# Performance work log

Measured on AMD Instinct MI355X. Metric: run time of the kernel, lower is better.

## Reference

```python
import jax, jax.numpy as jnp
import numpy as np

N_NODES = 50000
N_EDGES = 800000
F_IN = 128
HID = 128
N_CLASSES = 2
N_GRAPHS = 500
NEG_SLOPE = 0.2


def setup_inputs() -> dict:
    key = jax.random.key(0)
    ks = jax.random.split(key, 16)
    inp = {
        "x": jax.random.normal(ks[0], (N_NODES, F_IN), dtype=jnp.float32),
        "edge_index": jax.random.randint(ks[1], (2, N_EDGES), 0, N_NODES, dtype=jnp.int64),
        "batch": jnp.sort(jax.random.randint(ks[2], (N_NODES,), 0, N_GRAPHS, dtype=jnp.int64)),
    }
    dims = [(F_IN, HID), (HID, HID), (HID, HID)]
    for i, (din, dout) in enumerate(dims, start=1):
        s = 1.0 / np.sqrt(din)
        inp[f"W{i}"] = jax.random.uniform(ks[3 * i], (din, dout), minval=-s, maxval=s, dtype=jnp.float32)
        inp[f"a_src{i}"] = jax.random.uniform(ks[3 * i + 1], (dout,), minval=-s, maxval=s, dtype=jnp.float32)
        inp[f"a_dst{i}"] = jax.random.uniform(ks[3 * i + 2], (dout,), minval=-s, maxval=s, dtype=jnp.float32)
        inp[f"b{i}"] = jnp.zeros((dout,), dtype=jnp.float32)
    s = 1.0 / np.sqrt(HID)
    inp["W_lin"] = jax.random.uniform(ks[12], (HID, N_CLASSES), minval=-s, maxval=s, dtype=jnp.float32)
    inp["b_lin"] = jax.random.uniform(ks[13], (N_CLASSES,), minval=-s, maxval=s, dtype=jnp.float32)
    return inp


def gat_conv(x, src, dst, W, a_src, a_dst, b, n_nodes):
    # single-head PyG GATConv (heads=1, concat), self-loops already in src/dst
    h = x @ W                                   # [N, dout]
    alpha_src = h @ a_src                       # [N]
    alpha_dst = h @ a_dst                       # [N]
    e = jax.nn.leaky_relu(alpha_src[src] + alpha_dst[dst], NEG_SLOPE)  # [E]
    # segment softmax over edges grouped by destination node
    m = jax.ops.segment_max(e, dst, num_segments=n_nodes)
    ex = jnp.exp(e - m[dst])
    denom = jax.ops.segment_sum(ex, dst, num_segments=n_nodes)
    alpha = ex / denom[dst]                     # [E]
    out = jax.ops.segment_sum(h[src] * alpha[:, None], dst, num_segments=n_nodes)
    return out + b


def reference(x, edge_index, batch, W1, a_src1, a_dst1, b1, W2, a_src2, a_dst2, b2,
              W3, a_src3, a_dst3, b3, W_lin, b_lin):
    n = x.shape[0]
    loops = jnp.arange(n, dtype=edge_index.dtype)
    src = jnp.concatenate([edge_index[0], loops])
    dst = jnp.concatenate([edge_index[1], loops])

    h = jax.nn.relu(gat_conv(x, src, dst, W1, a_src1, a_dst1, b1, n))
    h = jax.nn.relu(gat_conv(h, src, dst, W2, a_src2, a_dst2, b2, n))
    h = gat_conv(h, src, dst, W3, a_src3, a_dst3, b3, n)

    # global mean pool over graphs
    sums = jax.ops.segment_sum(h, batch, num_segments=N_GRAPHS)       # [G, HID]
    counts = jax.ops.segment_sum(jnp.ones((n,), h.dtype), batch, num_segments=N_GRAPHS)
    pooled = sums / jnp.maximum(counts, 1.0)[:, None]
    # dropout is identity in eval mode
    return pooled @ W_lin + b_lin
```

## Files before the change

### kernel.cpp

```cpp
#include <hip/hip_runtime.h>
#include <math.h>

#define N_NODES  50000
#define N_EDGES  800000
#define FDIM     128
#define N_GRAPHS 500
#define NEG_SLOPE 0.2f
#define EN_TOTAL (N_EDGES + N_NODES)
#define SCAN_NB ((N_NODES + 255) / 256)
#define GEMM_TILES (N_NODES / 16)

typedef short bf16x8 __attribute__((ext_vector_type(8)));
typedef float f32x4 __attribute__((ext_vector_type(4)));

static __device__ __forceinline__ float lrelu(float x) {
    return x >= 0.f ? x : NEG_SLOPE * x;
}
static __device__ __forceinline__ unsigned short f2bf(float v) {
    unsigned int u = __float_as_uint(v);
    u += 0x7fffu + ((u >> 16) & 1u);
    return (unsigned short)(u >> 16);
}
static __device__ __forceinline__ float bf2f(unsigned short s) {
    return __uint_as_float(((unsigned int)s) << 16);
}

__global__ __launch_bounds__(256) void prep_planes(
    const float* __restrict__ X, unsigned short* __restrict__ hi,
    unsigned short* __restrict__ lo)
{
    const int total = N_NODES * FDIM / 4;
    for (int i = blockIdx.x * 256 + threadIdx.x; i < total; i += gridDim.x * 256) {
        const float4 v = ((const float4*)X)[i];
        ushort4 h4, l4;
        h4.x = f2bf(v.x); l4.x = f2bf(v.x - bf2f(h4.x));
        h4.y = f2bf(v.y); l4.y = f2bf(v.y - bf2f(h4.y));
        h4.z = f2bf(v.z); l4.z = f2bf(v.z - bf2f(h4.z));
        h4.w = f2bf(v.w); l4.w = f2bf(v.w - bf2f(h4.w));
        ((ushort4*)hi)[i] = h4;
        ((ushort4*)lo)[i] = l4;
    }
}

__global__ __launch_bounds__(256) void prep_wt(
    const float* __restrict__ W0, const float* __restrict__ W1,
    const float* __restrict__ W2, unsigned short* __restrict__ WT)
{
    const float* W = (blockIdx.x == 0) ? W0 : (blockIdx.x == 1) ? W1 : W2;
    unsigned short* hi = WT + (size_t)blockIdx.x * 2 * FDIM * FDIM;
    unsigned short* lo = hi + FDIM * FDIM;
    for (int i = threadIdx.x; i < FDIM * FDIM; i += 256) {
        const int k = i >> 7, c = i & 127;
        const float v = W[i];
        const unsigned short h = f2bf(v);
        hi[c * FDIM + k] = h;
        lo[c * FDIM + k] = f2bf(v - bf2f(h));
    }
}

__global__ __launch_bounds__(256) void gemm_mfma3(
    const unsigned short* __restrict__ Ahi, const unsigned short* __restrict__ Alo,
    const unsigned short* __restrict__ WThi, const unsigned short* __restrict__ WTlo,
    const float* __restrict__ Avs, const float* __restrict__ Avd,
    unsigned short* __restrict__ Hb, float* __restrict__ asrcN, float* __restrict__ adstN)
{
    __shared__ float sps[4][16], spd[4][16];

    const int tid = threadIdx.x, wv = tid >> 6, lane = tid & 63;
    const int r16 = lane & 15, g = lane >> 4;
    const int t0 = wv * 2;

    bf16x8 bh[2][4], bl[2][4];
    float as_v[2], ad_v[2];
    #pragma unroll
    for (int tt = 0; tt < 2; ++tt) {
        const int c = (t0 + tt) * 16 + r16;
        as_v[tt] = Avs[c];
        ad_v[tt] = Avd[c];
        #pragma unroll
        for (int cc = 0; cc < 4; ++cc) {
            bh[tt][cc] = *(const bf16x8*)(WThi + c * FDIM + cc * 32 + 8 * g);
            bl[tt][cc] = *(const bf16x8*)(WTlo + c * FDIM + cc * 32 + 8 * g);
        }
    }

    for (int tile = blockIdx.x; tile < GEMM_TILES; tile += gridDim.x) {
        const int m0 = tile * 16;
        const size_t ra = (size_t)(m0 + r16) * FDIM;

        f32x4 acc0 = {0.f, 0.f, 0.f, 0.f}, acc1 = {0.f, 0.f, 0.f, 0.f};
        #pragma unroll
        for (int cc = 0; cc < 4; ++cc) {
            const int k0 = cc * 32 + 8 * g;
            const bf16x8 ah = *(const bf16x8*)(Ahi + ra + k0);
            const bf16x8 al = *(const bf16x8*)(Alo + ra + k0);
            acc0 = __builtin_amdgcn_mfma_f32_16x16x32_bf16(ah, bh[0][cc], acc0, 0, 0, 0);
            acc1 = __builtin_amdgcn_mfma_f32_16x16x32_bf16(ah, bh[1][cc], acc1, 0, 0, 0);
            acc0 = __builtin_amdgcn_mfma_f32_16x16x32_bf16(al, bh[0][cc], acc0, 0, 0, 0);
            acc1 = __builtin_amdgcn_mfma_f32_16x16x32_bf16(al, bh[1][cc], acc1, 0, 0, 0);
            acc0 = __builtin_amdgcn_mfma_f32_16x16x32_bf16(ah, bl[0][cc], acc0, 0, 0, 0);
            acc1 = __builtin_amdgcn_mfma_f32_16x16x32_bf16(ah, bl[1][cc], acc1, 0, 0, 0);
        }

        float ps[4], pd[4];
        const int rowb = m0 + 4 * g;
        #pragma unroll
        for (int r = 0; r < 4; ++r) {
            const float h0 = acc0[r], h1 = acc1[r];
            Hb[(size_t)(rowb + r) * FDIM + (t0 + 0) * 16 + r16] = f2bf(h0);
            Hb[(size_t)(rowb + r) * FDIM + (t0 + 1) * 16 + r16] = f2bf(h1);
            ps[r] = h0 * as_v[0] + h1 * as_v[1];
            pd[r] = h0 * ad_v[0] + h1 * ad_v[1];
        }
        #pragma unroll
        for (int o = 1; o <= 8; o <<= 1) {
            #pragma unroll
            for (int r = 0; r < 4; ++r) {
                ps[r] += __shfl_xor(ps[r], o);
                pd[r] += __shfl_xor(pd[r], o);
            }
        }
        if (r16 == 0) {
            #pragma unroll
            for (int r = 0; r < 4; ++r) {
                sps[wv][4 * g + r] = ps[r];
                spd[wv][4 * g + r] = pd[r];
            }
        }
        __syncthreads();
        if (tid < 16) {
            asrcN[m0 + tid] = sps[0][tid] + sps[1][tid] + sps[2][tid] + sps[3][tid];
        } else if (tid < 32) {
            const int r = tid - 16;
            adstN[m0 + r] = spd[0][r] + spd[1][r] + spd[2][r] + spd[3][r];
        }
        __syncthreads();
    }
}

__global__ void count_edges(const int* __restrict__ ei, int* __restrict__ cnt) {
    int i = blockIdx.x * 256 + threadIdx.x;
    if (i < EN_TOTAL) {
        int d = (i < N_EDGES) ? ei[N_EDGES + i] : (i - N_EDGES);
        atomicAdd(&cnt[d], 1);
    }
}

__global__ __launch_bounds__(256) void scan_block(const int* __restrict__ cnt,
                                                  int* __restrict__ off,
                                                  int* __restrict__ blockSums) {
    __shared__ int s[256];
    const int i = blockIdx.x * 256 + threadIdx.x;
    s[threadIdx.x] = (i < N_NODES) ? cnt[i] : 0;
    __syncthreads();
    #pragma unroll
    for (int d = 1; d < 256; d <<= 1) {
        int t = (threadIdx.x >= d) ? s[threadIdx.x - d] : 0;
        __syncthreads();
        s[threadIdx.x] += t;
        __syncthreads();
    }
    if (i < N_NODES) off[i + 1] = s[threadIdx.x];
    if (threadIdx.x == 255) blockSums[blockIdx.x] = s[255];
}

__global__ __launch_bounds__(256) void scan_sums(int* __restrict__ blockSums) {
    __shared__ int s[256];
    s[threadIdx.x] = (threadIdx.x < SCAN_NB) ? blockSums[threadIdx.x] : 0;
    __syncthreads();
    #pragma unroll
    for (int d = 1; d < 256; d <<= 1) {
        int t = (threadIdx.x >= d) ? s[threadIdx.x - d] : 0;
        __syncthreads();
        s[threadIdx.x] += t;
        __syncthreads();
    }
    if (threadIdx.x < SCAN_NB)
        blockSums[threadIdx.x] = (threadIdx.x == 0) ? 0 : s[threadIdx.x - 1];
}

__global__ __launch_bounds__(256) void add_base(int* __restrict__ off,
                                                const int* __restrict__ blockSums) {
    const int i = blockIdx.x * 256 + threadIdx.x;
    if (i < N_NODES) off[i + 1] += blockSums[blockIdx.x];
    if (i == 0) off[0] = 0;
}

__global__ void scatter_edges(const int* __restrict__ ei, const int* __restrict__ off,
                              int* __restrict__ cur, int* __restrict__ srcs) {
    int i = blockIdx.x * 256 + threadIdx.x;
    if (i < EN_TOTAL) {
        int s, d;
        if (i < N_EDGES) { s = ei[i]; d = ei[N_EDGES + i]; }
        else             { s = d = i - N_EDGES; }
        int p = off[d] + atomicAdd(&cur[d], 1);
        srcs[p] = s;
    }
}

__global__ __launch_bounds__(256) void gat_aggregate(
    const unsigned short* __restrict__ Hb, const int* __restrict__ off,
    const int* __restrict__ srcs,
    const float* __restrict__ asrcN, const float* __restrict__ adstN,
    const float* __restrict__ bias,
    unsigned short* __restrict__ PHI, unsigned short* __restrict__ PLO,
    float* __restrict__ OUTF, int mode)
{
    const int wave = threadIdx.x >> 6, lane = threadIdx.x & 63;
    const int grp = lane >> 3, fl = lane & 7;

    for (int n = blockIdx.x * 4 + wave; n < N_NODES; n += gridDim.x * 4) {
        const int s0 = off[n], s1 = off[n + 1];
        const int deg = s1 - s0;
        const float ad = adstN[n];

        float e_reg = -1e30f;
        float m = -1e30f;
        for (int j = s0 + lane; j < s1; j += 64) {
            float e = lrelu(asrcN[srcs[j]] + ad);
            if (j - s0 < 64) e_reg = e;
            m = fmaxf(m, e);
        }
        #pragma unroll
        for (int o = 32; o; o >>= 1) m = fmaxf(m, __shfl_xor(m, o));

        float4 a0 = {0,0,0,0}, a1 = {0,0,0,0}, a2 = {0,0,0,0}, a3 = {0,0,0,0};
        float dn = 0.f;
        const unsigned short* Hf = Hb + (size_t)fl * 16;
        for (int j = s0 + grp; j < s1; j += 8) {
            const int s = srcs[j];
            const float ex = (deg <= 64)
                ? __expf(__shfl(e_reg, j - s0) - m)
                : __expf(lrelu(asrcN[s] + ad) - m);
            dn += ex;
            const uint4* hp = (const uint4*)(Hf + (size_t)s * FDIM);
            const uint4 u0 = hp[0], u1 = hp[1];
            a0.x += ex * __uint_as_float(u0.x << 16);
            a0.y += ex * __uint_as_float(u0.x & 0xffff0000u);
            a0.z += ex * __uint_as_float(u0.y << 16);
            a0.w += ex * __uint_as_float(u0.y & 0xffff0000u);
            a1.x += ex * __uint_as_float(u0.z << 16);
            a1.y += ex * __uint_as_float(u0.z & 0xffff0000u);
            a1.z += ex * __uint_as_float(u0.w << 16);
            a1.w += ex * __uint_as_float(u0.w & 0xffff0000u);
            a2.x += ex * __uint_as_float(u1.x << 16);
            a2.y += ex * __uint_as_float(u1.x & 0xffff0000u);
            a2.z += ex * __uint_as_float(u1.y << 16);
            a2.w += ex * __uint_as_float(u1.y & 0xffff0000u);
            a3.x += ex * __uint_as_float(u1.z << 16);
            a3.y += ex * __uint_as_float(u1.z & 0xffff0000u);
            a3.z += ex * __uint_as_float(u1.w << 16);
            a3.w += ex * __uint_as_float(u1.w & 0xffff0000u);
        }

        #pragma unroll
        for (int o = 8; o <= 32; o <<= 1) {
            dn  += __shfl_xor(dn, o);
            a0.x += __shfl_xor(a0.x, o); a0.y += __shfl_xor(a0.y, o);
            a0.z += __shfl_xor(a0.z, o); a0.w += __shfl_xor(a0.w, o);
            a1.x += __shfl_xor(a1.x, o); a1.y += __shfl_xor(a1.y, o);
            a1.z += __shfl_xor(a1.z, o); a1.w += __shfl_xor(a1.w, o);
            a2.x += __shfl_xor(a2.x, o); a2.y += __shfl_xor(a2.y, o);
            a2.z += __shfl_xor(a2.z, o); a2.w += __shfl_xor(a2.w, o);
            a3.x += __shfl_xor(a3.x, o); a3.y += __shfl_xor(a3.y, o);
            a3.z += __shfl_xor(a3.z, o); a3.w += __shfl_xor(a3.w, o);
        }

        if (grp == 0) {
            const float rd = 1.f / dn;
            const float4* bp = (const float4*)(bias + fl * 16);
            float4 ov[4] = {a0, a1, a2, a3};
            #pragma unroll
            for (int q = 0; q < 4; ++q) {
                const float4 b4 = bp[q];
                float4 o4;
                o4.x = ov[q].x * rd + b4.x; o4.y = ov[q].y * rd + b4.y;
                o4.z = ov[q].z * rd + b4.z; o4.w = ov[q].w * rd + b4.w;
                if (mode == 0) {
                    o4.x = fmaxf(o4.x, 0.f); o4.y = fmaxf(o4.y, 0.f);
                    o4.z = fmaxf(o4.z, 0.f); o4.w = fmaxf(o4.w, 0.f);
                    ushort4 h4, l4;
                    h4.x = f2bf(o4.x); l4.x = f2bf(o4.x - bf2f(h4.x));
                    h4.y = f2bf(o4.y); l4.y = f2bf(o4.y - bf2f(h4.y));
                    h4.z = f2bf(o4.z); l4.z = f2bf(o4.z - bf2f(h4.z));
                    h4.w = f2bf(o4.w); l4.w = f2bf(o4.w - bf2f(h4.w));
                    const size_t base = (size_t)n * FDIM + fl * 16 + q * 4;
                    *(ushort4*)(PHI + base) = h4;
                    *(ushort4*)(PLO + base) = l4;
                } else {
                    *(float4*)(OUTF + (size_t)n * FDIM + fl * 16 + q * 4) = o4;
                }
            }
        }
    }
}

__global__ __launch_bounds__(256) void pool_linear2(
    const float* __restrict__ H, const int* __restrict__ batch,
    const float* __restrict__ Wlin, const float* __restrict__ blin,
    float* __restrict__ out)
{
    const int g = blockIdx.x, tid = threadIdx.x;
    const int rl = tid >> 5, fq = tid & 31;

    int a = 0, b = N_NODES;
    while (a < b) { int mid = (a + b) >> 1; if (batch[mid] < g) a = mid + 1; else b = mid; }
    const int lo = a;
    b = N_NODES;
    while (a < b) { int mid = (a + b) >> 1; if (batch[mid] <= g) a = mid + 1; else b = mid; }
    const int hi = a;

    float4 acc = {0.f, 0.f, 0.f, 0.f};
    for (int n = lo + rl; n < hi; n += 8) {
        const float4 v = *(const float4*)(H + (size_t)n * FDIM + fq * 4);
        acc.x += v.x; acc.y += v.y; acc.z += v.z; acc.w += v.w;
    }
    __shared__ float4 s[8][32];
    s[rl][fq] = acc;
    __syncthreads();

    if (tid < 32) {
        float4 t = s[0][fq];
        #pragma unroll
        for (int r = 1; r < 8; ++r) {
            const float4 v = s[r][fq];
            t.x += v.x; t.y += v.y; t.z += v.z; t.w += v.w;
        }
        const float inv = 1.f / fmaxf((float)(hi - lo), 1.f);
        t.x *= inv; t.y *= inv; t.z *= inv; t.w *= inv;
        float d0 = t.x * Wlin[(fq * 4 + 0) * 2 + 0] + t.y * Wlin[(fq * 4 + 1) * 2 + 0]
                 + t.z * Wlin[(fq * 4 + 2) * 2 + 0] + t.w * Wlin[(fq * 4 + 3) * 2 + 0];
        float d1 = t.x * Wlin[(fq * 4 + 0) * 2 + 1] + t.y * Wlin[(fq * 4 + 1) * 2 + 1]
                 + t.z * Wlin[(fq * 4 + 2) * 2 + 1] + t.w * Wlin[(fq * 4 + 3) * 2 + 1];
        #pragma unroll
        for (int o = 1; o <= 16; o <<= 1) {
            d0 += __shfl_xor(d0, o);
            d1 += __shfl_xor(d1, o);
        }
        if (fq == 0) {
            out[g * 2 + 0] = d0 + blin[0];
            out[g * 2 + 1] = d1 + blin[1];
        }
    }
}

extern "C" void kernel_launch(void* const* d_in, const int* in_sizes, int n_in,
                              void* d_out, int out_size, void* d_ws, size_t ws_size,
                              hipStream_t stream)
{
    const float* x     = (const float*)d_in[0];
    const int*   ei    = (const int*)d_in[1];
    const int*   batch = (const int*)d_in[2];
    const float* W[3]    = {(const float*)d_in[3],  (const float*)d_in[7],  (const float*)d_in[11]};
    const float* avs[3]  = {(const float*)d_in[4],  (const float*)d_in[8],  (const float*)d_in[12]};
    const float* avd[3]  = {(const float*)d_in[5],  (const float*)d_in[9],  (const float*)d_in[13]};
    const float* bias[3] = {(const float*)d_in[6],  (const float*)d_in[10], (const float*)d_in[14]};
    const float* Wlin = (const float*)d_in[15];
    const float* blin = (const float*)d_in[16];
    float* out = (float*)d_out;

    char* w = (char*)d_ws;
    unsigned short* Ahi = (unsigned short*)w; w += (size_t)N_NODES * FDIM * 2;
    unsigned short* Alo = (unsigned short*)w; w += (size_t)N_NODES * FDIM * 2;
    float* hOf = (float*)Ahi;
    unsigned short* Hb = (unsigned short*)w; w += (size_t)N_NODES * FDIM * 2;
    float* attn  = (float*)w; w += 2 * 200192;
    int*   off   = (int*)w;   w += 200192;
    int*   cnt   = (int*)w;   w += 200192;
    int*   bsum  = (int*)w;   w += 4096;
    int*   srcs  = (int*)w;   w += (size_t)EN_TOTAL * 4;
    unsigned short* WT = (unsigned short*)w; w += 3 * 2 * FDIM * FDIM * 2;
    float* asrcN = attn;
    float* adstN = attn + N_NODES;

    prep_planes<<<1024, 256, 0, stream>>>(x, Ahi, Alo);
    prep_wt<<<3, 256, 0, stream>>>(W[0], W[1], W[2], WT);

    hipMemsetAsync(cnt, 0, N_NODES * sizeof(int), stream);
    count_edges<<<(EN_TOTAL + 255) / 256, 256, 0, stream>>>(ei, cnt);
    scan_block<<<SCAN_NB, 256, 0, stream>>>(cnt, off, bsum);
    scan_sums<<<1, 256, 0, stream>>>(bsum);
    add_base<<<SCAN_NB, 256, 0, stream>>>(off, bsum);
    hipMemsetAsync(cnt, 0, N_NODES * sizeof(int), stream);
    scatter_edges<<<(EN_TOTAL + 255) / 256, 256, 0, stream>>>(ei, off, cnt, srcs);

    for (int l = 0; l < 3; ++l) {
        const unsigned short* WThi = WT + (size_t)l * 2 * FDIM * FDIM;
        const unsigned short* WTlo = WThi + FDIM * FDIM;
        gemm_mfma3<<<1024, 256, 0, stream>>>(Ahi, Alo, WThi, WTlo,
                                             avs[l], avd[l], Hb, asrcN, adstN);
        gat_aggregate<<<2048, 256, 0, stream>>>(Hb, off, srcs, asrcN, adstN, bias[l],
                                                Ahi, Alo, hOf, (l < 2) ? 0 : 1);
    }

    pool_linear2<<<N_GRAPHS, 256, 0, stream>>>(hOf, batch, Wlin, blin, out);
}
```

Measured before the change: 352.4 us.

## Fold attention vectors into GEMM as extra columns, drop block reduction and syncs

Precomputes W·a_src and W·a_dst in prep_wt and appends them as extra transposed weight columns (padded to 144). One wave per tile, rotated across tiles, computes the attention logits with an extra set of MFMAs. This replaces the shuffle reduction, the shared-memory partial sums and two __syncthreads per tile. The A fragments are also loaded up front. Reassociating the attention dot products through bf16 split planes changes rounding slightly, and the work is unbalanced across waves.

```diff
diff --git a/kernel.cpp b/kernel.cpp
--- a/kernel.cpp
+++ b/kernel.cpp
@@ -9,6 +9,7 @@
 #define EN_TOTAL (N_EDGES + N_NODES)
 #define SCAN_NB ((N_NODES + 255) / 256)
 #define GEMM_TILES (N_NODES / 16)
+#define WT_COLS 144
 
 typedef short bf16x8 __attribute__((ext_vector_type(8)));
 typedef float f32x4 __attribute__((ext_vector_type(4)));
@@ -44,97 +45,120 @@
 
 __global__ __launch_bounds__(256) void prep_wt(
     const float* __restrict__ W0, const float* __restrict__ W1,
-    const float* __restrict__ W2, unsigned short* __restrict__ WT)
-{
-    const float* W = (blockIdx.x == 0) ? W0 : (blockIdx.x == 1) ? W1 : W2;
-    unsigned short* hi = WT + (size_t)blockIdx.x * 2 * FDIM * FDIM;
-    unsigned short* lo = hi + FDIM * FDIM;
-    for (int i = threadIdx.x; i < FDIM * FDIM; i += 256) {
+    const float* __restrict__ W2,
+    const float* __restrict__ as0, const float* __restrict__ as1,
+    const float* __restrict__ as2,
+    const float* __restrict__ ad0, const float* __restrict__ ad1,
+    const float* __restrict__ ad2,
+    unsigned short* __restrict__ WT)
+{
+    const int l = blockIdx.x;
+    const float* W  = (l == 0) ? W0  : (l == 1) ? W1  : W2;
+    const float* As = (l == 0) ? as0 : (l == 1) ? as1 : as2;
+    const float* Ad = (l == 0) ? ad0 : (l == 1) ? ad1 : ad2;
+    unsigned short* hi = WT + (size_t)l * 2 * WT_COLS * FDIM;
+    unsigned short* lo = hi + WT_COLS * FDIM;
+    const int tid = threadIdx.x;
+
+    __shared__ float wa[256];
+    {
+        const int k = tid & 127;
+        const float* av = (tid < 128) ? As : Ad;
+        float s = 0.f;
+        for (int c = 0; c < 128; ++c) s += W[k * FDIM + c] * av[c];
+        wa[tid] = s;
+    }
+    __syncthreads();
+
+    for (int i = tid; i < FDIM * FDIM; i += 256) {
         const int k = i >> 7, c = i & 127;
         const float v = W[i];
         const unsigned short h = f2bf(v);
         hi[c * FDIM + k] = h;
         lo[c * FDIM + k] = f2bf(v - bf2f(h));
     }
-}
-
-__global__ __launch_bounds__(256) void gemm_mfma3(
+    for (int k = tid; k < FDIM; k += 256) {
+        const float vs = wa[k], vd = wa[128 + k];
+        const unsigned short hs = f2bf(vs), hd = f2bf(vd);
+        hi[128 * FDIM + k] = hs; lo[128 * FDIM + k] = f2bf(vs - bf2f(hs));
+        hi[129 * FDIM + k] = hd; lo[129 * FDIM + k] = f2bf(vd - bf2f(hd));
+    }
+    for (int i = tid; i < 14 * FDIM; i += 256) {
+        hi[130 * FDIM + i] = 0;
+        lo[130 * FDIM + i] = 0;
+    }
+}
+
+__global__ __launch_bounds__(256) void gemm_mfma4(
     const unsigned short* __restrict__ Ahi, const unsigned short* __restrict__ Alo,
     const unsigned short* __restrict__ WThi, const unsigned short* __restrict__ WTlo,
-    const float* __restrict__ Avs, const float* __restrict__ Avd,
     unsigned short* __restrict__ Hb, float* __restrict__ asrcN, float* __restrict__ adstN)
 {
-    __shared__ float sps[4][16], spd[4][16];
-
     const int tid = threadIdx.x, wv = tid >> 6, lane = tid & 63;
     const int r16 = lane & 15, g = lane >> 4;
     const int t0 = wv * 2;
 
     bf16x8 bh[2][4], bl[2][4];
-    float as_v[2], ad_v[2];
     #pragma unroll
     for (int tt = 0; tt < 2; ++tt) {
         const int c = (t0 + tt) * 16 + r16;
-        as_v[tt] = Avs[c];
-        ad_v[tt] = Avd[c];
         #pragma unroll
         for (int cc = 0; cc < 4; ++cc) {
             bh[tt][cc] = *(const bf16x8*)(WThi + c * FDIM + cc * 32 + 8 * g);
             bl[tt][cc] = *(const bf16x8*)(WTlo + c * FDIM + cc * 32 + 8 * g);
         }
     }
-
-    for (int tile = blockIdx.x; tile < GEMM_TILES; tile += gridDim.x) {
+    const unsigned short* WThiE = WThi + (128 + r16) * FDIM + 8 * g;
+    const unsigned short* WTloE = WTlo + (128 + r16) * FDIM + 8 * g;
+
+    int rot = 0;
+    for (int tile = blockIdx.x; tile < GEMM_TILES; tile += gridDim.x, ++rot) {
         const int m0 = tile * 16;
         const size_t ra = (size_t)(m0 + r16) * FDIM;
 
+        bf16x8 ah[4], al[4];
+        #pragma unroll
+        for (int cc = 0; cc < 4; ++cc) {
+            ah[cc] = *(const bf16x8*)(Ahi + ra + cc * 32 + 8 * g);
+            al[cc] = *(const bf16x8*)(Alo + ra + cc * 32 + 8 * g);
+        }
+
         f32x4 acc0 = {0.f, 0.f, 0.f, 0.f}, acc1 = {0.f, 0.f, 0.f, 0.f};
         #pragma unroll
         for (int cc = 0; cc < 4; ++cc) {
-            const int k0 = cc * 32 + 8 * g;
-            const bf16x8 ah = *(const bf16x8*)(Ahi + ra + k0);
-            const bf16x8 al = *(const bf16x8*)(Alo + ra + k0);
-            acc0 = __builtin_amdgcn_mfma_f32_16x16x32_bf16(ah, bh[0][cc], acc0, 0, 0, 0);
-            acc1 = __builtin_amdgcn_mfma_f32_16x16x32_bf16(ah, bh[1][cc], acc1, 0, 0, 0);
-            acc0 = __builtin_amdgcn_mfma_f32_16x16x32_bf16(al, bh[0][cc], acc0, 0, 0, 0);
-            acc1 = __builtin_amdgcn_mfma_f32_16x16x32_bf16(al, bh[1][cc], acc1, 0, 0, 0);
-            acc0 = __builtin_amdgcn_mfma_f32_16x16x32_bf16(ah, bl[0][cc], acc0, 0, 0, 0);
-            acc1 = __builtin_amdgcn_mfma_f32_16x16x32_bf16(ah, bl[1][cc], acc1, 0, 0, 0);
-        }
-
-        float ps[4], pd[4];
+            acc0 = __builtin_amdgcn_mfma_f32_16x16x32_bf16(ah[cc], bh[0][cc], acc0, 0, 0, 0);
+            acc1 = __builtin_amdgcn_mfma_f32_16x16x32_bf16(ah[cc], bh[1][cc], acc1, 0, 0, 0);
+            acc0 = __builtin_amdgcn_mfma_f32_16x16x32_bf16(al[cc], bh[0][cc], acc0, 0, 0, 0);
+            acc1 = __builtin_amdgcn_mfma_f32_16x16x32_bf16(al[cc], bh[1][cc], acc1, 0, 0, 0);
+            acc0 = __builtin_amdgcn_mfma_f32_16x16x32_bf16(ah[cc], bl[0][cc], acc0, 0, 0, 0);
+            acc1 = __builtin_amdgcn_mfma_f32_16x16x32_bf16(ah[cc], bl[1][cc], acc1, 0, 0, 0);
+        }
+
         const int rowb = m0 + 4 * g;
         #pragma unroll
         for (int r = 0; r < 4; ++r) {
-            const float h0 = acc0[r], h1 = acc1[r];
-            Hb[(size_t)(rowb + r) * FDIM + (t0 + 0) * 16 + r16] = f2bf(h0);
-            Hb[(size_t)(rowb + r) * FDIM + (t0 + 1) * 16 + r16] = f2bf(h1);
-            ps[r] = h0 * as_v[0] + h1 * as_v[1];
-            pd[r] = h0 * ad_v[0] + h1 * ad_v[1];
-        }
-        #pragma unroll
-        for (int o = 1; o <= 8; o <<= 1) {
+            Hb[(size_t)(rowb + r) * FDIM + (t0 + 0) * 16 + r16] = f2bf(acc0[r]);
+            Hb[(size_t)(rowb + r) * FDIM + (t0 + 1) * 16 + r16] = f2bf(acc1[r]);
+        }
+
+        if (wv == ((tile + rot) & 3)) {
+            f32x4 acce = {0.f, 0.f, 0.f, 0.f};
             #pragma unroll
-            for (int r = 0; r < 4; ++r) {
-                ps[r] += __shfl_xor(ps[r], o);
-                pd[r] += __shfl_xor(pd[r], o);
+            for (int cc = 0; cc < 4; ++cc) {
+                const bf16x8 bhe = *(const bf16x8*)(WThiE + cc * 32);
+                const bf16x8 ble = *(const bf16x8*)(WTloE + cc * 32);
+                acce = __builtin_amdgcn_mfma_f32_16x16x32_bf16(ah[cc], bhe, acce, 0, 0, 0);
+                acce = __builtin_amdgcn_mfma_f32_16x16x32_bf16(al[cc], bhe, acce, 0, 0, 0);
+                acce = __builtin_amdgcn_mfma_f32_16x16x32_bf16(ah[cc], ble, acce, 0, 0, 0);
             }
-        }
-        if (r16 == 0) {
-            #pragma unroll
-            for (int r = 0; r < 4; ++r) {
-                sps[wv][4 * g + r] = ps[r];
-                spd[wv][4 * g + r] = pd[r];
+            if (r16 == 0) {
+                #pragma unroll
+                for (int r = 0; r < 4; ++r) asrcN[rowb + r] = acce[r];
+            } else if (r16 == 1) {
+                #pragma unroll
+                for (int r = 0; r < 4; ++r) adstN[rowb + r] = acce[r];
             }
         }
-        __syncthreads();
-        if (tid < 16) {
-            asrcN[m0 + tid] = sps[0][tid] + sps[1][tid] + sps[2][tid] + sps[3][tid];
-        } else if (tid < 32) {
-            const int r = tid - 16;
-            adstN[m0 + r] = spd[0][r] + spd[1][r] + spd[2][r] + spd[3][r];
-        }
-        __syncthreads();
     }
 }
 
@@ -369,12 +393,14 @@
     int*   cnt   = (int*)w;   w += 200192;
     int*   bsum  = (int*)w;   w += 4096;
     int*   srcs  = (int*)w;   w += (size_t)EN_TOTAL * 4;
-    unsigned short* WT = (unsigned short*)w; w += 3 * 2 * FDIM * FDIM * 2;
+    unsigned short* WT = (unsigned short*)w; w += (size_t)3 * 2 * WT_COLS * FDIM * 2;
     float* asrcN = attn;
     float* adstN = attn + N_NODES;
 
     prep_planes<<<1024, 256, 0, stream>>>(x, Ahi, Alo);
-    prep_wt<<<3, 256, 0, stream>>>(W[0], W[1], W[2], WT);
+    prep_wt<<<3, 256, 0, stream>>>(W[0], W[1], W[2],
+                                   avs[0], avs[1], avs[2],
+                                   avd[0], avd[1], avd[2], WT);
 
     hipMemsetAsync(cnt, 0, N_NODES * sizeof(int), stream);
     count_edges<<<(EN_TOTAL + 255) / 256, 256, 0, stream>>>(ei, cnt);
@@ -385,10 +411,9 @@
     scatter_edges<<<(EN_TOTAL + 255) / 256, 256, 0, stream>>>(ei, off, cnt, srcs);
 
     for (int l = 0; l < 3; ++l) {
-        const unsigned short* WThi = WT + (size_t)l * 2 * FDIM * FDIM;
-        const unsigned short* WTlo = WThi + FDIM * FDIM;
-        gemm_mfma3<<<1024, 256, 0, stream>>>(Ahi, Alo, WThi, WTlo,
-                                             avs[l], avd[l], Hb, asrcN, adstN);
+        const unsigned short* WThi = WT + (size_t)l * 2 * WT_COLS * FDIM;
+        const unsigned short* WTlo = WThi + WT_COLS * FDIM;
+        gemm_mfma4<<<1024, 256, 0, stream>>>(Ahi, Alo, WThi, WTlo, Hb, asrcN, adstN);
         gat_aggregate<<<2048, 256, 0, stream>>>(Hb, off, srcs, asrcN, adstN, bias[l],
                                                 Ahi, Alo, hOf, (l < 2) ? 0 : 1);
     }
```

Result: no change. 355.9 us (+1.0%).
